# Optimization experiments

Measured on AMD Instinct MI355X. Metric: run time of the kernel, lower is better.

The kernel has to match this reference:

```python
import jax, jax.numpy as jnp
import numpy as np

N = 100000   # nodes
E = 3200000  # edges
F = 128      # input features
H1 = 128     # first_gcn_dimensions
H2 = 64      # second_gcn_dimensions
D1 = 64      # first_dense_neurons
D2 = 8       # second_dense_neurons
L = 10       # number_of_labels


def setup_inputs() -> dict:
    key = jax.random.key(0)
    ks = jax.random.split(key, 8)
    edges = jax.random.randint(ks[0], (2, E), 0, N)
    features = jax.random.normal(ks[1], (N, F), dtype=jnp.float32)
    s = lambda k, shape: jax.random.normal(k, shape, dtype=jnp.float32) * 0.05
    return dict(
        edges=edges, features=features,
        W1=s(ks[2], (F, H1)), b1=jnp.zeros((H1,), jnp.float32),
        W2=s(ks[3], (H1, H2)), b2=jnp.zeros((H2,), jnp.float32),
        Wf1=s(ks[4], (H2, D1)), bf1=jnp.zeros((D1,), jnp.float32),
        Wf2=s(ks[5], (D1, D2)), bf2=jnp.zeros((D2,), jnp.float32),
        Wl=s(ks[6], (H2 * D2, L)), bl=jnp.zeros((L,), jnp.float32),
    )


def gcn_conv(x, W, b, src, dst, n):
    # PyG GCNConv: x' = D^{-1/2} (A + I) D^{-1/2} (x W) + b  (self-loops already in src/dst)
    h = x @ W                                            # [N, out]
    deg = jax.ops.segment_sum(jnp.ones(dst.shape[0], x.dtype), dst, num_segments=n)
    dinv = jnp.where(deg > 0, jax.lax.rsqrt(deg), 0.0)   # deg^{-1/2}, 0 for isolated
    norm = dinv[src] * dinv[dst]                         # [E+N]
    agg = jax.ops.segment_sum(h[src] * norm[:, None], dst, num_segments=n)
    return agg + b


def reference(edges, features, W1, b1, W2, b2, Wf1, bf1, Wf2, bf2, Wl, bl):
    n = features.shape[0]
    loop = jnp.arange(n)
    src = jnp.concatenate([edges[0], loop])
    dst = jnp.concatenate([edges[1], loop])

    h1 = jax.nn.relu(gcn_conv(features, W1, b1, src, dst, n))  # [N, H1]
    h2 = gcn_conv(h1, W2, b2, src, dst, n)                     # [N, H2]

    a1 = jnp.tanh(h2 @ Wf1 + bf1)                              # [N, D1]
    att = jax.nn.softmax(a1 @ Wf2 + bf2, axis=0)               # softmax over nodes, [N, D2]

    graph_embedding = (att.T @ h2).reshape(1, -1)              # [1, D2*H2]
    P = att.T @ att - jnp.eye(att.shape[1], dtype=att.dtype)   # [D2, D2]
    penalty = jnp.sum(jnp.sqrt(jnp.sum(P * P, axis=1)))

    predictions = jax.nn.log_softmax(graph_embedding @ Wl + bl, axis=1)  # [1, L]
    return graph_embedding, penalty, predictions
```

## Files before the change

### kernel.cpp

```cpp
#include <hip/hip_runtime.h>
#include <hip/hip_bf16.h>
#include <math.h>

#define NNODES 100000
#define NEDGES 3200000
#define NBUK ((NNODES + 127) >> 7)
#define NCHUNK 256
#define EPC (NEDGES / NCHUNK)

typedef float floatx2 __attribute__((ext_vector_type(2)));
typedef float f32x4 __attribute__((ext_vector_type(4)));
typedef short bf16x8 __attribute__((ext_vector_type(8)));

__device__ __forceinline__ unsigned short f2bf(float x) {
    unsigned u = __float_as_uint(x);
    unsigned r = u + 0x7FFFu + ((u >> 16) & 1u);
    return (unsigned short)(r >> 16);
}

__device__ __forceinline__ void acc8_fp8(uint2 v, floatx2* a) {
    a[0] += __builtin_amdgcn_cvt_pk_f32_fp8(v.x, false);
    a[1] += __builtin_amdgcn_cvt_pk_f32_fp8(v.x, true);
    a[2] += __builtin_amdgcn_cvt_pk_f32_fp8(v.y, false);
    a[3] += __builtin_amdgcn_cvt_pk_f32_fp8(v.y, true);
}
__device__ __forceinline__ void acc4_fp8(unsigned v, floatx2* a) {
    a[0] += __builtin_amdgcn_cvt_pk_f32_fp8(v, false);
    a[1] += __builtin_amdgcn_cvt_pk_f32_fp8(v, true);
}

__global__ void prep_w_kernel(const float* __restrict__ W1, const float* __restrict__ W2,
                              unsigned short* __restrict__ Wt1, unsigned short* __restrict__ Wt2) {
    int i = blockIdx.x * 256 + threadIdx.x;
    if (i < 128 * 128) {
        int k = i >> 7, n = i & 127;
        Wt1[n * 128 + k] = f2bf(W1[i]);
    } else if (i < 128 * 128 + 128 * 64) {
        int j = i - 128 * 128;
        int k = j >> 6, n = j & 63;
        Wt2[n * 128 + k] = f2bf(W2[j]);
    }
}

__global__ __launch_bounds__(1024) void chunk_hist_kernel(const int* __restrict__ dst,
                                                          int* __restrict__ hist) {
    __shared__ int h[NBUK];
    int c = blockIdx.x, t = threadIdx.x;
    for (int i = t; i < NBUK; i += 1024) h[i] = 0;
    __syncthreads();
    const int4* d4 = (const int4*)(dst + c * EPC);
    for (int i = t; i < EPC / 4; i += 1024) {
        int4 d = d4[i];
        atomicAdd(&h[d.x >> 7], 1);
        atomicAdd(&h[d.y >> 7], 1);
        atomicAdd(&h[d.z >> 7], 1);
        atomicAdd(&h[d.w >> 7], 1);
    }
    __syncthreads();
    for (int i = t; i < NBUK; i += 1024)
        hist[c * NBUK + i] = h[i];
}

__global__ void col_scan_kernel(int* __restrict__ hist, int* __restrict__ btot) {
    int t = blockIdx.x * 256 + threadIdx.x;
    if (t >= NBUK) return;
    int run = 0;
    for (int c = 0; c < NCHUNK; c++) {
        int idx = c * NBUK + t;
        int v = hist[idx];
        hist[idx] = run;
        run += v;
    }
    btot[t] = run;
}

__global__ void bucket_scan_kernel(const int* __restrict__ btot, int* __restrict__ bstart,
                                   int* __restrict__ row_start, float* __restrict__ smalls) {
    __shared__ int s[1024];
    int t = threadIdx.x;
    if (t < 592) smalls[t] = 0.0f;
    int v = (t < NBUK) ? btot[t] : 0;
    s[t] = v;
    __syncthreads();
    for (int off = 1; off < 1024; off <<= 1) {
        int x = (t >= off) ? s[t - off] : 0;
        __syncthreads();
        s[t] += x;
        __syncthreads();
    }
    if (t < NBUK) bstart[t] = s[t] - v;
    if (t == 0) {
        bstart[NBUK] = NEDGES;
        row_start[NNODES] = NEDGES;
    }
}

__global__ __launch_bounds__(1024) void chunk_scatter_kernel(const int* __restrict__ src,
                                                             const int* __restrict__ dst,
                                                             const int* __restrict__ hist,
                                                             const int* __restrict__ bstart,
                                                             int* __restrict__ ebuk) {
    __shared__ int cur[NBUK];
    int c = blockIdx.x, t = threadIdx.x;
    for (int i = t; i < NBUK; i += 1024)
        cur[i] = bstart[i] + hist[c * NBUK + i];
    __syncthreads();
    const int4* s4 = (const int4*)(src + c * EPC);
    const int4* d4 = (const int4*)(dst + c * EPC);
    for (int i = t; i < EPC / 4; i += 1024) {
        int4 s = s4[i];
        int4 d = d4[i];
        int p0 = atomicAdd(&cur[d.x >> 7], 1);
        ebuk[p0] = s.x | ((d.x & 127) << 20);
        int p1 = atomicAdd(&cur[d.y >> 7], 1);
        ebuk[p1] = s.y | ((d.y & 127) << 20);
        int p2 = atomicAdd(&cur[d.z >> 7], 1);
        ebuk[p2] = s.z | ((d.z & 127) << 20);
        int p3 = atomicAdd(&cur[d.w >> 7], 1);
        ebuk[p3] = s.w | ((d.w & 127) << 20);
    }
}

__global__ __launch_bounds__(256) void build_kernel(const int* __restrict__ ebuk,
                                                    const int* __restrict__ bstart,
                                                    int* __restrict__ row_start,
                                                    float* __restrict__ dinv,
                                                    int* __restrict__ csr) {
    __shared__ int cnt[128];
    __shared__ int scn[128];
    __shared__ int cur[128];
    int b = blockIdx.x;
    int t = threadIdx.x;
    int s0 = bstart[b], s1 = bstart[b + 1];
    if (t < 128) cnt[t] = 0;
    __syncthreads();
    for (int i = s0 + t; i < s1; i += 256)
        atomicAdd(&cnt[(ebuk[i] >> 20) & 127], 1);
    __syncthreads();
    if (t < 128) scn[t] = cnt[t];
    __syncthreads();
#pragma unroll
    for (int off = 1; off < 128; off <<= 1) {
        int x = (t < 128 && t >= off) ? scn[t - off] : 0;
        __syncthreads();
        if (t < 128) scn[t] += x;
        __syncthreads();
    }
    int node = b * 128 + t;
    if (t < 128) {
        int rs = s0 + scn[t] - cnt[t];
        cur[t] = rs;
        if (node < NNODES) {
            row_start[node] = rs;
            dinv[node] = rsqrtf((float)cnt[t] + 1.0f);
        }
    }
    __syncthreads();
    for (int i = s0 + t; i < s1; i += 256) {
        int v = ebuk[i];
        int pos = atomicAdd(&cur[(v >> 20) & 127], 1);
        csr[pos] = v & 0xFFFFF;
    }
}

template <int KIN, int KOUT, bool ABF16>
__global__ __launch_bounds__(256) void gemm_mfma_kernel(const void* __restrict__ Av,
                                                        const unsigned short* __restrict__ Wt,
                                                        const float* __restrict__ rowscale,
                                                        unsigned char* __restrict__ stage) {
    constexpr int LDK = KIN + 8;
    constexpr int LDC = KOUT + 4;
    constexpr int SH_AB = (64 + KOUT) * LDK * 2;
    constexpr int SH_C  = 64 * LDC * 4;
    constexpr int SH = SH_AB > SH_C ? SH_AB : SH_C;
    __shared__ char shbuf[SH];
    unsigned short* As = (unsigned short*)shbuf;
    unsigned short* Ws = As + 64 * LDK;
    float* Cs = (float*)shbuf;
    int t = threadIdx.x;
    int block_row = blockIdx.x * 64;

    for (int idx = t; idx < KOUT * (KIN / 8); idx += 256) {
        int n = idx / (KIN / 8), c = idx % (KIN / 8);
        *(uint4*)(Ws + n * LDK + c * 8) = *(const uint4*)(Wt + n * KIN + c * 8);
    }
    if (ABF16) {
        const unsigned short* A = (const unsigned short*)Av;
        for (int idx = t; idx < 64 * (KIN / 8); idx += 256) {
            int r = idx / (KIN / 8), c = idx % (KIN / 8);
            uint4 v = make_uint4(0, 0, 0, 0);
            if (block_row + r < NNODES)
                v = *(const uint4*)(A + (size_t)(block_row + r) * KIN + c * 8);
            *(uint4*)(As + r * LDK + c * 8) = v;
        }
    } else {
        const float* A = (const float*)Av;
        for (int idx = t; idx < 64 * (KIN / 4); idx += 256) {
            int r = idx / (KIN / 4), c = idx % (KIN / 4);
            float4 v = make_float4(0.f, 0.f, 0.f, 0.f);
            if (block_row + r < NNODES)
                v = *(const float4*)(A + (size_t)(block_row + r) * KIN + c * 4);
            unsigned p0 = (unsigned)f2bf(v.x) | ((unsigned)f2bf(v.y) << 16);
            unsigned p1 = (unsigned)f2bf(v.z) | ((unsigned)f2bf(v.w) << 16);
            *(uint2*)(As + r * LDK + c * 4) = make_uint2(p0, p1);
        }
    }
    __syncthreads();

    int wv = t >> 6, lane = t & 63;
    int r0 = wv * 16;
    int m = lane & 15, q = lane >> 4;
    constexpr int NT = KOUT / 16;
    constexpr int KS = KIN / 32;
    f32x4 acc[NT];
#pragma unroll
    for (int nt = 0; nt < NT; nt++) acc[nt] = (f32x4)(0.f);
    bf16x8 afr[KS];
#pragma unroll
    for (int ks = 0; ks < KS; ks++)
        afr[ks] = *(bf16x8*)(As + (r0 + m) * LDK + ks * 32 + q * 8);
#pragma unroll
    for (int nt = 0; nt < NT; nt++) {
#pragma unroll
        for (int ks = 0; ks < KS; ks++) {
            bf16x8 b = *(bf16x8*)(Ws + (nt * 16 + m) * LDK + ks * 32 + q * 8);
            acc[nt] = __builtin_amdgcn_mfma_f32_16x16x32_bf16(afr[ks], b, acc[nt], 0, 0, 0);
        }
    }
    __syncthreads();
#pragma unroll
    for (int nt = 0; nt < NT; nt++)
#pragma unroll
        for (int j = 0; j < 4; j++)
            Cs[(r0 + q * 4 + j) * LDC + nt * 16 + m] = acc[nt][j];
    __syncthreads();
    for (int idx = t; idx < 64 * (KOUT / 4); idx += 256) {
        int r = idx / (KOUT / 4), c4 = idx % (KOUT / 4);
        int row = block_row + r;
        if (row < NNODES) {
            float4 v = *(float4*)(Cs + r * LDC + c4 * 4);
            float d = rowscale[row];
            int pk = __builtin_amdgcn_cvt_pk_fp8_f32(v.x * d, v.y * d, 0, false);
            pk = __builtin_amdgcn_cvt_pk_fp8_f32(v.z * d, v.w * d, pk, true);
            *(unsigned*)(stage + (size_t)row * KOUT + c4 * 4) = (unsigned)pk;
        }
    }
}

__global__ __launch_bounds__(256) void gather128_kernel(
    const unsigned char* __restrict__ hs, const int* __restrict__ row_start,
    const int* __restrict__ csr, const float* __restrict__ dinv,
    const float* __restrict__ bias, unsigned short* __restrict__ out) {
    int wave = threadIdx.x >> 6;
    int lane = threadIdx.x & 63;
    int n = blockIdx.x * 4 + wave;
    if (n >= NNODES) return;
    int g = lane >> 4;
    int c = lane & 15;
    unsigned boff = (unsigned)c << 3;
    int start = row_start[n], end = row_start[n + 1];
    floatx2 acc[4];
#pragma unroll
    for (int i = 0; i < 4; i++) acc[i] = (floatx2)(0.f);
    int w = (start + 3) & ~3;
    if (w > end) w = end;
    {
        int e2 = start + g;
        if (e2 < w) {
            unsigned o = ((unsigned)csr[e2] << 7) + boff;
            acc8_fp8(*(const uint2*)(hs + o), acc);
        }
    }
    for (; w + 32 <= end; w += 32) {
        int4 ca = *(const int4*)(csr + w + 4 * g);
        int4 cbv = *(const int4*)(csr + w + 16 + 4 * g);
        uint2 v0 = *(const uint2*)(hs + (((unsigned)ca.x  << 7) + boff));
        uint2 v1 = *(const uint2*)(hs + (((unsigned)ca.y  << 7) + boff));
        uint2 v2 = *(const uint2*)(hs + (((unsigned)ca.z  << 7) + boff));
        uint2 v3 = *(const uint2*)(hs + (((unsigned)ca.w  << 7) + boff));
        uint2 v4 = *(const uint2*)(hs + (((unsigned)cbv.x << 7) + boff));
        uint2 v5 = *(const uint2*)(hs + (((unsigned)cbv.y << 7) + boff));
        uint2 v6 = *(const uint2*)(hs + (((unsigned)cbv.z << 7) + boff));
        uint2 v7 = *(const uint2*)(hs + (((unsigned)cbv.w << 7) + boff));
        acc8_fp8(v0, acc); acc8_fp8(v1, acc); acc8_fp8(v2, acc); acc8_fp8(v3, acc);
        acc8_fp8(v4, acc); acc8_fp8(v5, acc); acc8_fp8(v6, acc); acc8_fp8(v7, acc);
    }
    for (; w + 16 <= end; w += 16) {
        int4 cs = *(const int4*)(csr + w + 4 * g);
        uint2 v0 = *(const uint2*)(hs + (((unsigned)cs.x << 7) + boff));
        uint2 v1 = *(const uint2*)(hs + (((unsigned)cs.y << 7) + boff));
        uint2 v2 = *(const uint2*)(hs + (((unsigned)cs.z << 7) + boff));
        uint2 v3 = *(const uint2*)(hs + (((unsigned)cs.w << 7) + boff));
        acc8_fp8(v0, acc); acc8_fp8(v1, acc); acc8_fp8(v2, acc); acc8_fp8(v3, acc);
    }
    for (int e2 = w + g; e2 < end; e2 += 4) {
        unsigned o = ((unsigned)csr[e2] << 7) + boff;
        acc8_fp8(*(const uint2*)(hs + o), acc);
    }
#pragma unroll
    for (int off = 16; off <= 32; off <<= 1)
#pragma unroll
        for (int i = 0; i < 4; i++) {
            acc[i].x += __shfl_xor(acc[i].x, off);
            acc[i].y += __shfl_xor(acc[i].y, off);
        }
    if (g == 0) {
        floatx2 s[4];
#pragma unroll
        for (int i = 0; i < 4; i++) s[i] = (floatx2)(0.f);
        acc8_fp8(*(const uint2*)(hs + (((unsigned)n << 7) + boff)), s);
        float d = dinv[n];
        int j = c * 8;
        float4 b0 = *(const float4*)(bias + j);
        float4 b1 = *(const float4*)(bias + j + 4);
        float r0 = fmaxf((acc[0].x + s[0].x) * d + b0.x, 0.f);
        float r1 = fmaxf((acc[0].y + s[0].y) * d + b0.y, 0.f);
        float r2 = fmaxf((acc[1].x + s[1].x) * d + b0.z, 0.f);
        float r3 = fmaxf((acc[1].y + s[1].y) * d + b0.w, 0.f);
        float r4 = fmaxf((acc[2].x + s[2].x) * d + b1.x, 0.f);
        float r5 = fmaxf((acc[2].y + s[2].y) * d + b1.y, 0.f);
        float r6 = fmaxf((acc[3].x + s[3].x) * d + b1.z, 0.f);
        float r7 = fmaxf((acc[3].y + s[3].y) * d + b1.w, 0.f);
        uint4 p;
        p.x = (unsigned)f2bf(r0) | ((unsigned)f2bf(r1) << 16);
        p.y = (unsigned)f2bf(r2) | ((unsigned)f2bf(r3) << 16);
        p.z = (unsigned)f2bf(r4) | ((unsigned)f2bf(r5) << 16);
        p.w = (unsigned)f2bf(r6) | ((unsigned)f2bf(r7) << 16);
        *(uint4*)(out + (((size_t)n << 7) + j)) = p;
    }
}

__global__ __launch_bounds__(256) void gather64_kernel(
    const unsigned char* __restrict__ hs, const int* __restrict__ row_start,
    const int* __restrict__ csr, const float* __restrict__ dinv,
    const float* __restrict__ bias, float* __restrict__ out) {
    int wave = threadIdx.x >> 6;
    int lane = threadIdx.x & 63;
    int n = blockIdx.x * 4 + wave;
    if (n >= NNODES) return;
    int g = lane >> 4;
    int c = lane & 15;
    unsigned boff = (unsigned)c << 2;
    int start = row_start[n], end = row_start[n + 1];
    floatx2 acc[2];
    acc[0] = (floatx2)(0.f); acc[1] = (floatx2)(0.f);
    int w = (start + 3) & ~3;
    if (w > end) w = end;
    {
        int e2 = start + g;
        if (e2 < w) {
            unsigned o = ((unsigned)csr[e2] << 6) + boff;
            acc4_fp8(*(const unsigned*)(hs + o), acc);
        }
    }
    for (; w + 32 <= end; w += 32) {
        int4 ca = *(const int4*)(csr + w + 4 * g);
        int4 cbv = *(const int4*)(csr + w + 16 + 4 * g);
        unsigned v0 = *(const unsigned*)(hs + (((unsigned)ca.x  << 6) + boff));
        unsigned v1 = *(const unsigned*)(hs + (((unsigned)ca.y  << 6) + boff));
        unsigned v2 = *(const unsigned*)(hs + (((unsigned)ca.z  << 6) + boff));
        unsigned v3 = *(const unsigned*)(hs + (((unsigned)ca.w  << 6) + boff));
        unsigned v4 = *(const unsigned*)(hs + (((unsigned)cbv.x << 6) + boff));
        unsigned v5 = *(const unsigned*)(hs + (((unsigned)cbv.y << 6) + boff));
        unsigned v6 = *(const unsigned*)(hs + (((unsigned)cbv.z << 6) + boff));
        unsigned v7 = *(const unsigned*)(hs + (((unsigned)cbv.w << 6) + boff));
        acc4_fp8(v0, acc); acc4_fp8(v1, acc); acc4_fp8(v2, acc); acc4_fp8(v3, acc);
        acc4_fp8(v4, acc); acc4_fp8(v5, acc); acc4_fp8(v6, acc); acc4_fp8(v7, acc);
    }
    for (; w + 16 <= end; w += 16) {
        int4 cs = *(const int4*)(csr + w + 4 * g);
        unsigned v0 = *(const unsigned*)(hs + (((unsigned)cs.x << 6) + boff));
        unsigned v1 = *(const unsigned*)(hs + (((unsigned)cs.y << 6) + boff));
        unsigned v2 = *(const unsigned*)(hs + (((unsigned)cs.z << 6) + boff));
        unsigned v3 = *(const unsigned*)(hs + (((unsigned)cs.w << 6) + boff));
        acc4_fp8(v0, acc); acc4_fp8(v1, acc); acc4_fp8(v2, acc); acc4_fp8(v3, acc);
    }
    for (int e2 = w + g; e2 < end; e2 += 4) {
        unsigned o = ((unsigned)csr[e2] << 6) + boff;
        acc4_fp8(*(const unsigned*)(hs + o), acc);
    }
#pragma unroll
    for (int off = 16; off <= 32; off <<= 1)
#pragma unroll
        for (int i = 0; i < 2; i++) {
            acc[i].x += __shfl_xor(acc[i].x, off);
            acc[i].y += __shfl_xor(acc[i].y, off);
        }
    if (g == 0) {
        floatx2 s[2];
        s[0] = (floatx2)(0.f); s[1] = (floatx2)(0.f);
        acc4_fp8(*(const unsigned*)(hs + (((unsigned)n << 6) + boff)), s);
        float d = dinv[n];
        int j = c * 4;
        float4 b4 = *(const float4*)(bias + j);
        float4 r;
        r.x = (acc[0].x + s[0].x) * d + b4.x;
        r.y = (acc[0].y + s[0].y) * d + b4.y;
        r.z = (acc[1].x + s[1].x) * d + b4.z;
        r.w = (acc[1].y + s[1].y) * d + b4.w;
        *(float4*)(out + (((size_t)n << 6) + j)) = r;
    }
}

__global__ __launch_bounds__(256) void attnpool_kernel(const float* __restrict__ h2,
                                                       const float* __restrict__ Wf1,
                                                       const float* __restrict__ bf1,
                                                       const float* __restrict__ Wf2,
                                                       const float* __restrict__ bf2,
                                                       float* __restrict__ ge,
                                                       float* __restrict__ ata,
                                                       float* __restrict__ colsum) {
    __shared__ float h2S[64][68];
    __shared__ float a1S[64][68];
    __shared__ float attS[64][8];
    __shared__ float colS[8][64];
    int t = threadIdx.x;
    int d0 = t >> 6;
    int j  = t & 63;
    int de = t >> 3, ee = t & 7;
    float accge0 = 0.f, accge1 = 0.f, accata = 0.f, acccol = 0.f;
    int ntiles = (NNODES + 63) / 64;
    for (int tile = blockIdx.x; tile < ntiles; tile += gridDim.x) {
        int base = tile * 64;
#pragma unroll
        for (int q = 0; q < 4; q++) {
            int idx = t + q * 256;
            int r = idx >> 4, cc = (idx & 15) * 4;
            int row = base + r;
            float4 v = (row < NNODES) ? *(const float4*)(h2 + (size_t)row * 64 + cc)
                                      : make_float4(0.f, 0.f, 0.f, 0.f);
            *(float4*)(&h2S[r][cc]) = v;
        }
        __syncthreads();
        {
            int cg = t & 15, rg = t >> 4;
            int jj = cg * 4, r0 = rg * 4;
            float4 b4 = *(const float4*)(bf1 + jj);
            float4 acc[4];
#pragma unroll
            for (int r = 0; r < 4; r++) acc[r] = b4;
#pragma unroll 4
            for (int k = 0; k < 64; k++) {
                float4 wv = *(const float4*)(Wf1 + (size_t)k * 64 + jj);
#pragma unroll
                for (int r = 0; r < 4; r++) {
                    float a = h2S[r0 + r][k];
                    acc[r].x += a * wv.x; acc[r].y += a * wv.y;
                    acc[r].z += a * wv.z; acc[r].w += a * wv.w;
                }
            }
#pragma unroll
            for (int r = 0; r < 4; r++) {
                a1S[r0 + r][jj]     = tanhf(acc[r].x);
                a1S[r0 + r][jj + 1] = tanhf(acc[r].y);
                a1S[r0 + r][jj + 2] = tanhf(acc[r].z);
                a1S[r0 + r][jj + 3] = tanhf(acc[r].w);
            }
        }
        __syncthreads();
        {
            int cc = t & 7, r = t >> 3;
#pragma unroll
            for (int h = 0; h < 2; h++) {
                int rr = r + h * 32;
                float acc = bf2[cc];
                for (int k = 0; k < 64; k++)
                    acc += a1S[rr][k] * Wf2[(size_t)k * 8 + cc];
                float ev = (base + rr < NNODES) ? __expf(acc) : 0.f;
                attS[rr][cc] = ev;
                colS[cc][rr] = ev;
            }
        }
        __syncthreads();
#pragma unroll 8
        for (int i = 0; i < 64; i++) {
            float hv = h2S[i][j];
            accge0 += attS[i][d0] * hv;
            accge1 += attS[i][d0 + 4] * hv;
        }
        if (t < 64) {
#pragma unroll 8
            for (int i = 0; i < 64; i++) accata += attS[i][de] * attS[i][ee];
        }
        if (t < 8) {
            float s = 0.f;
#pragma unroll
            for (int r = 0; r < 64; r++) s += colS[t][r];
            acccol += s;
        }
        __syncthreads();
    }
    atomicAdd(ge + d0 * 64 + j, accge0);
    atomicAdd(ge + (d0 + 4) * 64 + j, accge1);
    if (t < 64) atomicAdd(ata + de * 8 + ee, accata);
    if (t < 8) atomicAdd(colsum + t, acccol);
}

__global__ void final_kernel(const float* __restrict__ geacc, const float* __restrict__ ata,
                             const float* __restrict__ colsum, const float* __restrict__ Wl,
                             const float* __restrict__ bl, float* __restrict__ out) {
    __shared__ float geF[512];
    __shared__ float inv[8];
    __shared__ float logits[10];
    int t = threadIdx.x;
    if (t < 8) inv[t] = 1.0f / colsum[t];
    __syncthreads();
    for (int idx = t; idx < 512; idx += 64) {
        int d = idx >> 6;
        float v = geacc[idx] * inv[d];
        geF[idx] = v;
        out[idx] = v;
    }
    __syncthreads();
    if (t == 0) {
        float pen = 0.f;
        for (int d = 0; d < 8; d++) {
            float s = 0.f;
            for (int e = 0; e < 8; e++) {
                float p = ata[d * 8 + e] * inv[d] * inv[e] - (d == e ? 1.0f : 0.0f);
                s += p * p;
            }
            pen += sqrtf(s);
        }
        out[512] = pen;
    }
    if (t < 10) {
        float acc = bl[t];
        for (int k = 0; k < 512; k++) acc += geF[k] * Wl[(size_t)k * 10 + t];
        logits[t] = acc;
    }
    __syncthreads();
    if (t == 0) {
        float m = -INFINITY;
        for (int l = 0; l < 10; l++) m = fmaxf(m, logits[l]);
        float s = 0.f;
        for (int l = 0; l < 10; l++) s += expf(logits[l] - m);
        float ls = logf(s);
        for (int l = 0; l < 10; l++) out[513 + l] = logits[l] - m - ls;
    }
}

extern "C" void kernel_launch(void* const* d_in, const int* in_sizes, int n_in,
                              void* d_out, int out_size, void* d_ws, size_t ws_size,
                              hipStream_t stream) {
    const int* esrc = (const int*)d_in[0];
    const int* edst = esrc + NEDGES;
    const float* X   = (const float*)d_in[1];
    const float* W1  = (const float*)d_in[2];
    const float* b1  = (const float*)d_in[3];
    const float* W2  = (const float*)d_in[4];
    const float* b2  = (const float*)d_in[5];
    const float* Wf1 = (const float*)d_in[6];
    const float* bf1 = (const float*)d_in[7];
    const float* Wf2 = (const float*)d_in[8];
    const float* bf2 = (const float*)d_in[9];
    const float* Wl  = (const float*)d_in[10];
    const float* bl  = (const float*)d_in[11];
    float* out = (float*)d_out;

    float* ws     = (float*)d_ws;
    float* dinv   = ws;
    float* smalls = ws + 100352;
    float* colsum = smalls + 8;
    float* ata    = smalls + 16;
    float* geacc  = smalls + 80;
    float* A = ws + 101376;
    float* B = A + (size_t)NNODES * 128;
    int* row_start = (int*)(B + (size_t)NNODES * 128);
    int* btot      = row_start + 100352;
    int* bstart    = btot + 1024;
    int* csr       = bstart + 1024;
    unsigned short* Wt1 = (unsigned short*)(csr + NEDGES);
    unsigned short* Wt2 = Wt1 + 128 * 128;
    int* ebuk      = (int*)A;
    int* hist      = (int*)B;
    unsigned char* stage = (unsigned char*)A;
    unsigned short* h1 = (unsigned short*)B;
    float* h2  = B;

    prep_w_kernel<<<96, 256, 0, stream>>>(W1, W2, Wt1, Wt2);

    chunk_hist_kernel<<<NCHUNK, 1024, 0, stream>>>(edst, hist);
    col_scan_kernel<<<4, 256, 0, stream>>>(hist, btot);
    bucket_scan_kernel<<<1, 1024, 0, stream>>>(btot, bstart, row_start, smalls);
    chunk_scatter_kernel<<<NCHUNK, 1024, 0, stream>>>(esrc, edst, hist, bstart, ebuk);
    build_kernel<<<NBUK, 256, 0, stream>>>(ebuk, bstart, row_start, dinv, csr);

    gemm_mfma_kernel<128, 128, false><<<(NNODES + 63) / 64, 256, 0, stream>>>(X, Wt1, dinv, stage);
    gather128_kernel<<<(NNODES + 3) / 4, 256, 0, stream>>>(stage, row_start, csr, dinv, b1, h1);

    gemm_mfma_kernel<128, 64, true><<<(NNODES + 63) / 64, 256, 0, stream>>>(h1, Wt2, dinv, stage);
    gather64_kernel<<<(NNODES + 3) / 4, 256, 0, stream>>>(stage, row_start, csr, dinv, b2, h2);

    attnpool_kernel<<<512, 256, 0, stream>>>(h2, Wf1, bf1, Wf2, bf2, geacc, ata, colsum);
    final_kernel<<<1, 64, 0, stream>>>(geacc, ata, colsum, Wl, bl, out);
}
```

Baseline: 430.9 us.

## Fuse gathers with downstream GEMM and attention pooling, merge prep and scan kernels

The layer-1 neighbor gather now runs inside the layer-2 GEMM kernel, writing the ReLU bf16 rows straight into shared memory instead of round-tripping h1 through global memory. The layer-2 gather is folded into the attention-pooling kernel, so the fp32 h2 tensor is never materialized. The weight-prep kernel is merged into the histogram kernel as extra blocks, and the column and bucket scans are combined into one kernel, cutting launches. The cost is less parallelism in the gathers: each wave now handles 16 rows in sequence instead of one node, which may hurt latency hiding for the irregular loads.

```diff
diff --git a/kernel.cpp b/kernel.cpp
--- a/kernel.cpp
+++ b/kernel.cpp
@@ -29,23 +29,26 @@
     a[1] += __builtin_amdgcn_cvt_pk_f32_fp8(v, true);
 }
 
-__global__ void prep_w_kernel(const float* __restrict__ W1, const float* __restrict__ W2,
-                              unsigned short* __restrict__ Wt1, unsigned short* __restrict__ Wt2) {
-    int i = blockIdx.x * 256 + threadIdx.x;
-    if (i < 128 * 128) {
-        int k = i >> 7, n = i & 127;
-        Wt1[n * 128 + k] = f2bf(W1[i]);
-    } else if (i < 128 * 128 + 128 * 64) {
-        int j = i - 128 * 128;
-        int k = j >> 6, n = j & 63;
-        Wt2[n * 128 + k] = f2bf(W2[j]);
-    }
-}
-
-__global__ __launch_bounds__(1024) void chunk_hist_kernel(const int* __restrict__ dst,
-                                                          int* __restrict__ hist) {
+__global__ __launch_bounds__(1024) void hist_prep_kernel(const int* __restrict__ dst,
+                                                         int* __restrict__ hist,
+                                                         const float* __restrict__ W1,
+                                                         const float* __restrict__ W2,
+                                                         unsigned short* __restrict__ Wt1,
+                                                         unsigned short* __restrict__ Wt2) {
+    int c = blockIdx.x, t = threadIdx.x;
+    if (c >= NCHUNK) {
+        int i = (c - NCHUNK) * 1024 + t;
+        if (i < 128 * 128) {
+            int k = i >> 7, n = i & 127;
+            Wt1[n * 128 + k] = f2bf(W1[i]);
+        } else {
+            int j = i - 128 * 128;
+            int k = j >> 6, n = j & 63;
+            Wt2[n * 128 + k] = f2bf(W2[j]);
+        }
+        return;
+    }
     __shared__ int h[NBUK];
-    int c = blockIdx.x, t = threadIdx.x;
     for (int i = t; i < NBUK; i += 1024) h[i] = 0;
     __syncthreads();
     const int4* d4 = (const int4*)(dst + c * EPC);
@@ -61,26 +64,22 @@
         hist[c * NBUK + i] = h[i];
 }
 
-__global__ void col_scan_kernel(int* __restrict__ hist, int* __restrict__ btot) {
-    int t = blockIdx.x * 256 + threadIdx.x;
-    if (t >= NBUK) return;
-    int run = 0;
-    for (int c = 0; c < NCHUNK; c++) {
-        int idx = c * NBUK + t;
-        int v = hist[idx];
-        hist[idx] = run;
-        run += v;
-    }
-    btot[t] = run;
-}
-
-__global__ void bucket_scan_kernel(const int* __restrict__ btot, int* __restrict__ bstart,
-                                   int* __restrict__ row_start, float* __restrict__ smalls) {
+__global__ __launch_bounds__(1024) void scan_kernel(int* __restrict__ hist, int* __restrict__ bstart,
+                                                    int* __restrict__ row_start,
+                                                    float* __restrict__ smalls) {
     __shared__ int s[1024];
     int t = threadIdx.x;
     if (t < 592) smalls[t] = 0.0f;
-    int v = (t < NBUK) ? btot[t] : 0;
-    s[t] = v;
+    int run = 0;
+    if (t < NBUK) {
+        for (int c = 0; c < NCHUNK; c++) {
+            int idx = c * NBUK + t;
+            int v = hist[idx];
+            hist[idx] = run;
+            run += v;
+        }
+    }
+    s[t] = (t < NBUK) ? run : 0;
     __syncthreads();
     for (int off = 1; off < 1024; off <<= 1) {
         int x = (t >= off) ? s[t - off] : 0;
@@ -88,7 +87,7 @@
         s[t] += x;
         __syncthreads();
     }
-    if (t < NBUK) bstart[t] = s[t] - v;
+    if (t < NBUK) bstart[t] = s[t] - run;
     if (t == 0) {
         bstart[NBUK] = NEDGES;
         row_start[NNODES] = NEDGES;
@@ -163,11 +162,11 @@
     }
 }
 
-template <int KIN, int KOUT, bool ABF16>
-__global__ __launch_bounds__(256) void gemm_mfma_kernel(const void* __restrict__ Av,
-                                                        const unsigned short* __restrict__ Wt,
-                                                        const float* __restrict__ rowscale,
-                                                        unsigned char* __restrict__ stage) {
+__global__ __launch_bounds__(256) void gemm1_mfma_kernel(const float* __restrict__ A,
+                                                         const unsigned short* __restrict__ Wt,
+                                                         const float* __restrict__ rowscale,
+                                                         unsigned char* __restrict__ stage) {
+    constexpr int KIN = 128, KOUT = 128;
     constexpr int LDK = KIN + 8;
     constexpr int LDC = KOUT + 4;
     constexpr int SH_AB = (64 + KOUT) * LDK * 2;
@@ -184,26 +183,14 @@
         int n = idx / (KIN / 8), c = idx % (KIN / 8);
         *(uint4*)(Ws + n * LDK + c * 8) = *(const uint4*)(Wt + n * KIN + c * 8);
     }
-    if (ABF16) {
-        const unsigned short* A = (const unsigned short*)Av;
-        for (int idx = t; idx < 64 * (KIN / 8); idx += 256) {
-            int r = idx / (KIN / 8), c = idx % (KIN / 8);
-            uint4 v = make_uint4(0, 0, 0, 0);
-            if (block_row + r < NNODES)
-                v = *(const uint4*)(A + (size_t)(block_row + r) * KIN + c * 8);
-            *(uint4*)(As + r * LDK + c * 8) = v;
-        }
-    } else {
-        const float* A = (const float*)Av;
-        for (int idx = t; idx < 64 * (KIN / 4); idx += 256) {
-            int r = idx / (KIN / 4), c = idx % (KIN / 4);
-            float4 v = make_float4(0.f, 0.f, 0.f, 0.f);
-            if (block_row + r < NNODES)
-                v = *(const float4*)(A + (size_t)(block_row + r) * KIN + c * 4);
-            unsigned p0 = (unsigned)f2bf(v.x) | ((unsigned)f2bf(v.y) << 16);
-            unsigned p1 = (unsigned)f2bf(v.z) | ((unsigned)f2bf(v.w) << 16);
-            *(uint2*)(As + r * LDK + c * 4) = make_uint2(p0, p1);
-        }
+    for (int idx = t; idx < 64 * (KIN / 4); idx += 256) {
+        int r = idx / (KIN / 4), c = idx % (KIN / 4);
+        float4 v = make_float4(0.f, 0.f, 0.f, 0.f);
+        if (block_row + r < NNODES)
+            v = *(const float4*)(A + (size_t)(block_row + r) * KIN + c * 4);
+        unsigned p0 = (unsigned)f2bf(v.x) | ((unsigned)f2bf(v.y) << 16);
+        unsigned p1 = (unsigned)f2bf(v.z) | ((unsigned)f2bf(v.w) << 16);
+        *(uint2*)(As + r * LDK + c * 4) = make_uint2(p0, p1);
     }
     __syncthreads();
 
@@ -247,189 +234,236 @@
     }
 }
 
-__global__ __launch_bounds__(256) void gather128_kernel(
+__global__ __launch_bounds__(256) void g128_gemm2_kernel(
     const unsigned char* __restrict__ hs, const int* __restrict__ row_start,
     const int* __restrict__ csr, const float* __restrict__ dinv,
-    const float* __restrict__ bias, unsigned short* __restrict__ out) {
-    int wave = threadIdx.x >> 6;
-    int lane = threadIdx.x & 63;
-    int n = blockIdx.x * 4 + wave;
-    if (n >= NNODES) return;
-    int g = lane >> 4;
-    int c = lane & 15;
-    unsigned boff = (unsigned)c << 3;
-    int start = row_start[n], end = row_start[n + 1];
-    floatx2 acc[4];
-#pragma unroll
-    for (int i = 0; i < 4; i++) acc[i] = (floatx2)(0.f);
-    int w = (start + 3) & ~3;
-    if (w > end) w = end;
+    const float* __restrict__ b1, const unsigned short* __restrict__ Wt2,
+    unsigned char* __restrict__ stage2) {
+    constexpr int KIN = 128, KOUT = 64;
+    constexpr int LDK = KIN + 8;
+    constexpr int LDC = KOUT + 4;
+    __shared__ unsigned short As[64 * LDK];
+    __shared__ unsigned short Ws[KOUT * LDK];
+    float* Cs = (float*)As;
+    int t = threadIdx.x;
+    int block_row = blockIdx.x * 64;
+    int wv = t >> 6, lane = t & 63;
+
+    for (int idx = t; idx < KOUT * (KIN / 8); idx += 256) {
+        int n = idx / (KIN / 8), cc = idx % (KIN / 8);
+        *(uint4*)(Ws + n * LDK + cc * 8) = *(const uint4*)(Wt2 + n * KIN + cc * 8);
+    }
     {
-        int e2 = start + g;
-        if (e2 < w) {
-            unsigned o = ((unsigned)csr[e2] << 7) + boff;
-            acc8_fp8(*(const uint2*)(hs + o), acc);
-        }
-    }
-    for (; w + 32 <= end; w += 32) {
-        int4 ca = *(const int4*)(csr + w + 4 * g);
-        int4 cbv = *(const int4*)(csr + w + 16 + 4 * g);
-        uint2 v0 = *(const uint2*)(hs + (((unsigned)ca.x  << 7) + boff));
-        uint2 v1 = *(const uint2*)(hs + (((unsigned)ca.y  << 7) + boff));
-        uint2 v2 = *(const uint2*)(hs + (((unsigned)ca.z  << 7) + boff));
-        uint2 v3 = *(const uint2*)(hs + (((unsigned)ca.w  << 7) + boff));
-        uint2 v4 = *(const uint2*)(hs + (((unsigned)cbv.x << 7) + boff));
-        uint2 v5 = *(const uint2*)(hs + (((unsigned)cbv.y << 7) + boff));
-        uint2 v6 = *(const uint2*)(hs + (((unsigned)cbv.z << 7) + boff));
-        uint2 v7 = *(const uint2*)(hs + (((unsigned)cbv.w << 7) + boff));
-        acc8_fp8(v0, acc); acc8_fp8(v1, acc); acc8_fp8(v2, acc); acc8_fp8(v3, acc);
-        acc8_fp8(v4, acc); acc8_fp8(v5, acc); acc8_fp8(v6, acc); acc8_fp8(v7, acc);
-    }
-    for (; w + 16 <= end; w += 16) {
-        int4 cs = *(const int4*)(csr + w + 4 * g);
-        uint2 v0 = *(const uint2*)(hs + (((unsigned)cs.x << 7) + boff));
-        uint2 v1 = *(const uint2*)(hs + (((unsigned)cs.y << 7) + boff));
-        uint2 v2 = *(const uint2*)(hs + (((unsigned)cs.z << 7) + boff));
-        uint2 v3 = *(const uint2*)(hs + (((unsigned)cs.w << 7) + boff));
-        acc8_fp8(v0, acc); acc8_fp8(v1, acc); acc8_fp8(v2, acc); acc8_fp8(v3, acc);
-    }
-    for (int e2 = w + g; e2 < end; e2 += 4) {
-        unsigned o = ((unsigned)csr[e2] << 7) + boff;
-        acc8_fp8(*(const uint2*)(hs + o), acc);
-    }
-#pragma unroll
-    for (int off = 16; off <= 32; off <<= 1)
-#pragma unroll
-        for (int i = 0; i < 4; i++) {
-            acc[i].x += __shfl_xor(acc[i].x, off);
-            acc[i].y += __shfl_xor(acc[i].y, off);
-        }
-    if (g == 0) {
-        floatx2 s[4];
-#pragma unroll
-        for (int i = 0; i < 4; i++) s[i] = (floatx2)(0.f);
-        acc8_fp8(*(const uint2*)(hs + (((unsigned)n << 7) + boff)), s);
-        float d = dinv[n];
-        int j = c * 8;
-        float4 b0 = *(const float4*)(bias + j);
-        float4 b1 = *(const float4*)(bias + j + 4);
-        float r0 = fmaxf((acc[0].x + s[0].x) * d + b0.x, 0.f);
-        float r1 = fmaxf((acc[0].y + s[0].y) * d + b0.y, 0.f);
-        float r2 = fmaxf((acc[1].x + s[1].x) * d + b0.z, 0.f);
-        float r3 = fmaxf((acc[1].y + s[1].y) * d + b0.w, 0.f);
-        float r4 = fmaxf((acc[2].x + s[2].x) * d + b1.x, 0.f);
-        float r5 = fmaxf((acc[2].y + s[2].y) * d + b1.y, 0.f);
-        float r6 = fmaxf((acc[3].x + s[3].x) * d + b1.z, 0.f);
-        float r7 = fmaxf((acc[3].y + s[3].y) * d + b1.w, 0.f);
-        uint4 p;
-        p.x = (unsigned)f2bf(r0) | ((unsigned)f2bf(r1) << 16);
-        p.y = (unsigned)f2bf(r2) | ((unsigned)f2bf(r3) << 16);
-        p.z = (unsigned)f2bf(r4) | ((unsigned)f2bf(r5) << 16);
-        p.w = (unsigned)f2bf(r6) | ((unsigned)f2bf(r7) << 16);
-        *(uint4*)(out + (((size_t)n << 7) + j)) = p;
-    }
-}
-
-__global__ __launch_bounds__(256) void gather64_kernel(
+        int g = lane >> 4, c = lane & 15;
+        unsigned boff = (unsigned)c << 3;
+        for (int i = 0; i < 16; i++) {
+            int r = wv * 16 + i;
+            int n = block_row + r;
+            if (n >= NNODES) {
+                if (g == 0) *(uint4*)(As + r * LDK + c * 8) = make_uint4(0, 0, 0, 0);
+                continue;
+            }
+            int start = row_start[n], end = row_start[n + 1];
+            floatx2 acc[4];
+#pragma unroll
+            for (int ii = 0; ii < 4; ii++) acc[ii] = (floatx2)(0.f);
+            int w = (start + 3) & ~3;
+            if (w > end) w = end;
+            {
+                int e2 = start + g;
+                if (e2 < w) {
+                    unsigned o = ((unsigned)csr[e2] << 7) + boff;
+                    acc8_fp8(*(const uint2*)(hs + o), acc);
+                }
+            }
+            for (; w + 32 <= end; w += 32) {
+                int4 ca = *(const int4*)(csr + w + 4 * g);
+                int4 cbv = *(const int4*)(csr + w + 16 + 4 * g);
+                uint2 v0 = *(const uint2*)(hs + (((unsigned)ca.x  << 7) + boff));
+                uint2 v1 = *(const uint2*)(hs + (((unsigned)ca.y  << 7) + boff));
+                uint2 v2 = *(const uint2*)(hs + (((unsigned)ca.z  << 7) + boff));
+                uint2 v3 = *(const uint2*)(hs + (((unsigned)ca.w  << 7) + boff));
+                uint2 v4 = *(const uint2*)(hs + (((unsigned)cbv.x << 7) + boff));
+                uint2 v5 = *(const uint2*)(hs + (((unsigned)cbv.y << 7) + boff));
+                uint2 v6 = *(const uint2*)(hs + (((unsigned)cbv.z << 7) + boff));
+                uint2 v7 = *(const uint2*)(hs + (((unsigned)cbv.w << 7) + boff));
+                acc8_fp8(v0, acc); acc8_fp8(v1, acc); acc8_fp8(v2, acc); acc8_fp8(v3, acc);
+                acc8_fp8(v4, acc); acc8_fp8(v5, acc); acc8_fp8(v6, acc); acc8_fp8(v7, acc);
+            }
+            for (; w + 16 <= end; w += 16) {
+                int4 cs = *(const int4*)(csr + w + 4 * g);
+                uint2 v0 = *(const uint2*)(hs + (((unsigned)cs.x << 7) + boff));
+                uint2 v1 = *(const uint2*)(hs + (((unsigned)cs.y << 7) + boff));
+                uint2 v2 = *(const uint2*)(hs + (((unsigned)cs.z << 7) + boff));
+                uint2 v3 = *(const uint2*)(hs + (((unsigned)cs.w << 7) + boff));
+                acc8_fp8(v0, acc); acc8_fp8(v1, acc); acc8_fp8(v2, acc); acc8_fp8(v3, acc);
+            }
+            for (int e2 = w + g; e2 < end; e2 += 4) {
+                unsigned o = ((unsigned)csr[e2] << 7) + boff;
+                acc8_fp8(*(const uint2*)(hs + o), acc);
+            }
+#pragma unroll
+            for (int off = 16; off <= 32; off <<= 1)
+#pragma unroll
+                for (int ii = 0; ii < 4; ii++) {
+                    acc[ii].x += __shfl_xor(acc[ii].x, off);
+                    acc[ii].y += __shfl_xor(acc[ii].y, off);
+                }
+            if (g == 0) {
+                floatx2 s[4];
+#pragma unroll
+                for (int ii = 0; ii < 4; ii++) s[ii] = (floatx2)(0.f);
+                acc8_fp8(*(const uint2*)(hs + (((unsigned)n << 7) + boff)), s);
+                float d = dinv[n];
+                int j = c * 8;
+                float4 bb0 = *(const float4*)(b1 + j);
+                float4 bb1 = *(const float4*)(b1 + j + 4);
+                float r0 = fmaxf((acc[0].x + s[0].x) * d + bb0.x, 0.f);
+                float r1 = fmaxf((acc[0].y + s[0].y) * d + bb0.y, 0.f);
+                float r2 = fmaxf((acc[1].x + s[1].x) * d + bb0.z, 0.f);
+                float r3 = fmaxf((acc[1].y + s[1].y) * d + bb0.w, 0.f);
+                float r4 = fmaxf((acc[2].x + s[2].x) * d + bb1.x, 0.f);
+                float r5 = fmaxf((acc[2].y + s[2].y) * d + bb1.y, 0.f);
+                float r6 = fmaxf((acc[3].x + s[3].x) * d + bb1.z, 0.f);
+                float r7 = fmaxf((acc[3].y + s[3].y) * d + bb1.w, 0.f);
+                uint4 p;
+                p.x = (unsigned)f2bf(r0) | ((unsigned)f2bf(r1) << 16);
+                p.y = (unsigned)f2bf(r2) | ((unsigned)f2bf(r3) << 16);
+                p.z = (unsigned)f2bf(r4) | ((unsigned)f2bf(r5) << 16);
+                p.w = (unsigned)f2bf(r6) | ((unsigned)f2bf(r7) << 16);
+                *(uint4*)(As + r * LDK + c * 8) = p;
+            }
+        }
+    }
+    __syncthreads();
+    int r0 = wv * 16;
+    int m = lane & 15, q = lane >> 4;
+    constexpr int NT = KOUT / 16;
+    constexpr int KS = KIN / 32;
+    f32x4 acc[NT];
+#pragma unroll
+    for (int nt = 0; nt < NT; nt++) acc[nt] = (f32x4)(0.f);
+    bf16x8 afr[KS];
+#pragma unroll
+    for (int ks = 0; ks < KS; ks++)
+        afr[ks] = *(bf16x8*)(As + (r0 + m) * LDK + ks * 32 + q * 8);
+#pragma unroll
+    for (int nt = 0; nt < NT; nt++) {
+#pragma unroll
+        for (int ks = 0; ks < KS; ks++) {
+            bf16x8 b = *(bf16x8*)(Ws + (nt * 16 + m) * LDK + ks * 32 + q * 8);
+            acc[nt] = __builtin_amdgcn_mfma_f32_16x16x32_bf16(afr[ks], b, acc[nt], 0, 0, 0);
+        }
+    }
+    __syncthreads();
+#pragma unroll
+    for (int nt = 0; nt < NT; nt++)
+#pragma unroll
+        for (int j = 0; j < 4; j++)
+            Cs[(r0 + q * 4 + j) * LDC + nt * 16 + m] = acc[nt][j];
+    __syncthreads();
+    for (int idx = t; idx < 64 * (KOUT / 4); idx += 256) {
+        int r = idx / (KOUT / 4), c4 = idx % (KOUT / 4);
+        int row = block_row + r;
+        if (row < NNODES) {
+            float4 v = *(float4*)(Cs + r * LDC + c4 * 4);
+            float d = dinv[row];
+            int pk = __builtin_amdgcn_cvt_pk_fp8_f32(v.x * d, v.y * d, 0, false);
+            pk = __builtin_amdgcn_cvt_pk_fp8_f32(v.z * d, v.w * d, pk, true);
+            *(unsigned*)(stage2 + (size_t)row * KOUT + c4 * 4) = (unsigned)pk;
+        }
+    }
+}
+
+__global__ __launch_bounds__(256) void g64_attnpool_kernel(
     const unsigned char* __restrict__ hs, const int* __restrict__ row_start,
     const int* __restrict__ csr, const float* __restrict__ dinv,
-    const float* __restrict__ bias, float* __restrict__ out) {
-    int wave = threadIdx.x >> 6;
-    int lane = threadIdx.x & 63;
-    int n = blockIdx.x * 4 + wave;
-    if (n >= NNODES) return;
-    int g = lane >> 4;
-    int c = lane & 15;
-    unsigned boff = (unsigned)c << 2;
-    int start = row_start[n], end = row_start[n + 1];
-    floatx2 acc[2];
-    acc[0] = (floatx2)(0.f); acc[1] = (floatx2)(0.f);
-    int w = (start + 3) & ~3;
-    if (w > end) w = end;
-    {
-        int e2 = start + g;
-        if (e2 < w) {
-            unsigned o = ((unsigned)csr[e2] << 6) + boff;
-            acc4_fp8(*(const unsigned*)(hs + o), acc);
-        }
-    }
-    for (; w + 32 <= end; w += 32) {
-        int4 ca = *(const int4*)(csr + w + 4 * g);
-        int4 cbv = *(const int4*)(csr + w + 16 + 4 * g);
-        unsigned v0 = *(const unsigned*)(hs + (((unsigned)ca.x  << 6) + boff));
-        unsigned v1 = *(const unsigned*)(hs + (((unsigned)ca.y  << 6) + boff));
-        unsigned v2 = *(const unsigned*)(hs + (((unsigned)ca.z  << 6) + boff));
-        unsigned v3 = *(const unsigned*)(hs + (((unsigned)ca.w  << 6) + boff));
-        unsigned v4 = *(const unsigned*)(hs + (((unsigned)cbv.x << 6) + boff));
-        unsigned v5 = *(const unsigned*)(hs + (((unsigned)cbv.y << 6) + boff));
-        unsigned v6 = *(const unsigned*)(hs + (((unsigned)cbv.z << 6) + boff));
-        unsigned v7 = *(const unsigned*)(hs + (((unsigned)cbv.w << 6) + boff));
-        acc4_fp8(v0, acc); acc4_fp8(v1, acc); acc4_fp8(v2, acc); acc4_fp8(v3, acc);
-        acc4_fp8(v4, acc); acc4_fp8(v5, acc); acc4_fp8(v6, acc); acc4_fp8(v7, acc);
-    }
-    for (; w + 16 <= end; w += 16) {
-        int4 cs = *(const int4*)(csr + w + 4 * g);
-        unsigned v0 = *(const unsigned*)(hs + (((unsigned)cs.x << 6) + boff));
-        unsigned v1 = *(const unsigned*)(hs + (((unsigned)cs.y << 6) + boff));
-        unsigned v2 = *(const unsigned*)(hs + (((unsigned)cs.z << 6) + boff));
-        unsigned v3 = *(const unsigned*)(hs + (((unsigned)cs.w << 6) + boff));
-        acc4_fp8(v0, acc); acc4_fp8(v1, acc); acc4_fp8(v2, acc); acc4_fp8(v3, acc);
-    }
-    for (int e2 = w + g; e2 < end; e2 += 4) {
-        unsigned o = ((unsigned)csr[e2] << 6) + boff;
-        acc4_fp8(*(const unsigned*)(hs + o), acc);
-    }
-#pragma unroll
-    for (int off = 16; off <= 32; off <<= 1)
-#pragma unroll
-        for (int i = 0; i < 2; i++) {
-            acc[i].x += __shfl_xor(acc[i].x, off);
-            acc[i].y += __shfl_xor(acc[i].y, off);
-        }
-    if (g == 0) {
-        floatx2 s[2];
-        s[0] = (floatx2)(0.f); s[1] = (floatx2)(0.f);
-        acc4_fp8(*(const unsigned*)(hs + (((unsigned)n << 6) + boff)), s);
-        float d = dinv[n];
-        int j = c * 4;
-        float4 b4 = *(const float4*)(bias + j);
-        float4 r;
-        r.x = (acc[0].x + s[0].x) * d + b4.x;
-        r.y = (acc[0].y + s[0].y) * d + b4.y;
-        r.z = (acc[1].x + s[1].x) * d + b4.z;
-        r.w = (acc[1].y + s[1].y) * d + b4.w;
-        *(float4*)(out + (((size_t)n << 6) + j)) = r;
-    }
-}
-
-__global__ __launch_bounds__(256) void attnpool_kernel(const float* __restrict__ h2,
-                                                       const float* __restrict__ Wf1,
-                                                       const float* __restrict__ bf1,
-                                                       const float* __restrict__ Wf2,
-                                                       const float* __restrict__ bf2,
-                                                       float* __restrict__ ge,
-                                                       float* __restrict__ ata,
-                                                       float* __restrict__ colsum) {
+    const float* __restrict__ b2,
+    const float* __restrict__ Wf1, const float* __restrict__ bf1,
+    const float* __restrict__ Wf2, const float* __restrict__ bf2,
+    float* __restrict__ ge, float* __restrict__ ata, float* __restrict__ colsum) {
     __shared__ float h2S[64][68];
     __shared__ float a1S[64][68];
     __shared__ float attS[64][8];
     __shared__ float colS[8][64];
     int t = threadIdx.x;
-    int d0 = t >> 6;
-    int j  = t & 63;
+    int wv = t >> 6, lane = t & 63;
+    int d0 = t >> 6, j = t & 63;
     int de = t >> 3, ee = t & 7;
     float accge0 = 0.f, accge1 = 0.f, accata = 0.f, acccol = 0.f;
     int ntiles = (NNODES + 63) / 64;
     for (int tile = blockIdx.x; tile < ntiles; tile += gridDim.x) {
         int base = tile * 64;
-#pragma unroll
-        for (int q = 0; q < 4; q++) {
-            int idx = t + q * 256;
-            int r = idx >> 4, cc = (idx & 15) * 4;
-            int row = base + r;
-            float4 v = (row < NNODES) ? *(const float4*)(h2 + (size_t)row * 64 + cc)
-                                      : make_float4(0.f, 0.f, 0.f, 0.f);
-            *(float4*)(&h2S[r][cc]) = v;
+        {
+            int g = lane >> 4, c = lane & 15;
+            unsigned boff = (unsigned)c << 2;
+            for (int i = 0; i < 16; i++) {
+                int r = wv * 16 + i;
+                int n = base + r;
+                if (n >= NNODES) {
+                    if (g == 0) *(float4*)(&h2S[r][c * 4]) = make_float4(0.f, 0.f, 0.f, 0.f);
+                    continue;
+                }
+                int start = row_start[n], end = row_start[n + 1];
+                floatx2 acc[2];
+                acc[0] = (floatx2)(0.f); acc[1] = (floatx2)(0.f);
+                int w = (start + 3) & ~3;
+                if (w > end) w = end;
+                {
+                    int e2 = start + g;
+                    if (e2 < w) {
+                        unsigned o = ((unsigned)csr[e2] << 6) + boff;
+                        acc4_fp8(*(const unsigned*)(hs + o), acc);
+                    }
+                }
+                for (; w + 32 <= end; w += 32) {
+                    int4 ca = *(const int4*)(csr + w + 4 * g);
+                    int4 cbv = *(const int4*)(csr + w + 16 + 4 * g);
+                    unsigned v0 = *(const unsigned*)(hs + (((unsigned)ca.x  << 6) + boff));
+                    unsigned v1 = *(const unsigned*)(hs + (((unsigned)ca.y  << 6) + boff));
+                    unsigned v2 = *(const unsigned*)(hs + (((unsigned)ca.z  << 6) + boff));
+                    unsigned v3 = *(const unsigned*)(hs + (((unsigned)ca.w  << 6) + boff));
+                    unsigned v4 = *(const unsigned*)(hs + (((unsigned)cbv.x << 6) + boff));
+                    unsigned v5 = *(const unsigned*)(hs + (((unsigned)cbv.y << 6) + boff));
+                    unsigned v6 = *(const unsigned*)(hs + (((unsigned)cbv.z << 6) + boff));
+                    unsigned v7 = *(const unsigned*)(hs + (((unsigned)cbv.w << 6) + boff));
+                    acc4_fp8(v0, acc); acc4_fp8(v1, acc); acc4_fp8(v2, acc); acc4_fp8(v3, acc);
+                    acc4_fp8(v4, acc); acc4_fp8(v5, acc); acc4_fp8(v6, acc); acc4_fp8(v7, acc);
+                }
+                for (; w + 16 <= end; w += 16) {
+                    int4 cs = *(const int4*)(csr + w + 4 * g);
+                    unsigned v0 = *(const unsigned*)(hs + (((unsigned)cs.x << 6) + boff));
+                    unsigned v1 = *(const unsigned*)(hs + (((unsigned)cs.y << 6) + boff));
+                    unsigned v2 = *(const unsigned*)(hs + (((unsigned)cs.z << 6) + boff));
+                    unsigned v3 = *(const unsigned*)(hs + (((unsigned)cs.w << 6) + boff));
+                    acc4_fp8(v0, acc); acc4_fp8(v1, acc); acc4_fp8(v2, acc); acc4_fp8(v3, acc);
+                }
+                for (int e2 = w + g; e2 < end; e2 += 4) {
+                    unsigned o = ((unsigned)csr[e2] << 6) + boff;
+                    acc4_fp8(*(const unsigned*)(hs + o), acc);
+                }
+#pragma unroll
+                for (int off = 16; off <= 32; off <<= 1)
+#pragma unroll
+                    for (int ii = 0; ii < 2; ii++) {
+                        acc[ii].x += __shfl_xor(acc[ii].x, off);
+                        acc[ii].y += __shfl_xor(acc[ii].y, off);
+                    }
+                if (g == 0) {
+                    floatx2 s[2];
+                    s[0] = (floatx2)(0.f); s[1] = (floatx2)(0.f);
+                    acc4_fp8(*(const unsigned*)(hs + (((unsigned)n << 6) + boff)), s);
+                    float d = dinv[n];
+                    int jj = c * 4;
+                    float4 b4 = *(const float4*)(b2 + jj);
+                    float4 res;
+                    res.x = (acc[0].x + s[0].x) * d + b4.x;
+                    res.y = (acc[0].y + s[0].y) * d + b4.y;
+                    res.z = (acc[1].x + s[1].x) * d + b4.z;
+                    res.w = (acc[1].y + s[1].y) * d + b4.w;
+                    *(float4*)(&h2S[r][jj]) = res;
+                }
+            }
         }
         __syncthreads();
         {
@@ -441,12 +475,12 @@
             for (int r = 0; r < 4; r++) acc[r] = b4;
 #pragma unroll 4
             for (int k = 0; k < 64; k++) {
-                float4 wv = *(const float4*)(Wf1 + (size_t)k * 64 + jj);
+                float4 wv4 = *(const float4*)(Wf1 + (size_t)k * 64 + jj);
 #pragma unroll
                 for (int r = 0; r < 4; r++) {
                     float a = h2S[r0 + r][k];
-                    acc[r].x += a * wv.x; acc[r].y += a * wv.y;
-                    acc[r].z += a * wv.z; acc[r].w += a * wv.w;
+                    acc[r].x += a * wv4.x; acc[r].y += a * wv4.y;
+                    acc[r].z += a * wv4.z; acc[r].w += a * wv4.w;
                 }
             }
 #pragma unroll
@@ -567,31 +601,26 @@
     float* A = ws + 101376;
     float* B = A + (size_t)NNODES * 128;
     int* row_start = (int*)(B + (size_t)NNODES * 128);
-    int* btot      = row_start + 100352;
-    int* bstart    = btot + 1024;
+    int* bstart    = row_start + 100352;
     int* csr       = bstart + 1024;
     unsigned short* Wt1 = (unsigned short*)(csr + NEDGES);
     unsigned short* Wt2 = Wt1 + 128 * 128;
     int* ebuk      = (int*)A;
     int* hist      = (int*)B;
-    unsigned char* stage = (unsigned char*)A;
-    unsigned short* h1 = (unsigned short*)B;
-    float* h2  = B;
-
-    prep_w_kernel<<<96, 256, 0, stream>>>(W1, W2, Wt1, Wt2);
-
-    chunk_hist_kernel<<<NCHUNK, 1024, 0, stream>>>(edst, hist);
-    col_scan_kernel<<<4, 256, 0, stream>>>(hist, btot);
-    bucket_scan_kernel<<<1, 1024, 0, stream>>>(btot, bstart, row_start, smalls);
+    unsigned char* stage1 = (unsigned char*)A;
+    unsigned char* stage2 = (unsigned char*)B;
+
+    hist_prep_kernel<<<NCHUNK + 24, 1024, 0, stream>>>(edst, hist, W1, W2, Wt1, Wt2);
+    scan_kernel<<<1, 1024, 0, stream>>>(hist, bstart, row_start, smalls);
     chunk_scatter_kernel<<<NCHUNK, 1024, 0, stream>>>(esrc, edst, hist, bstart, ebuk);
     build_kernel<<<NBUK, 256, 0, stream>>>(ebuk, bstart, row_start, dinv, csr);
 
-    gemm_mfma_kernel<128, 128, false><<<(NNODES + 63) / 64, 256, 0, stream>>>(X, Wt1, dinv, stage);
-    gather128_kernel<<<(NNODES + 3) / 4, 256, 0, stream>>>(stage, row_start, csr, dinv, b1, h1);
-
-    gemm_mfma_kernel<128, 64, true><<<(NNODES + 63) / 64, 256, 0, stream>>>(h1, Wt2, dinv, stage);
-    gather64_kernel<<<(NNODES + 3) / 4, 256, 0, stream>>>(stage, row_start, csr, dinv, b2, h2);
-
-    attnpool_kernel<<<512, 256, 0, stream>>>(h2, Wf1, bf1, Wf2, bf2, geacc, ata, colsum);
+    gemm1_mfma_kernel<<<(NNODES + 63) / 64, 256, 0, stream>>>(X, Wt1, dinv, stage1);
+
+    g128_gemm2_kernel<<<(NNODES + 63) / 64, 256, 0, stream>>>(stage1, row_start, csr, dinv,
+                                                              b1, Wt2, stage2);
+
+    g64_attnpool_kernel<<<782, 256, 0, stream>>>(stage2, row_start, csr, dinv, b2,
+                                                 Wf1, bf1, Wf2, bf2, geacc, ata, colsum);
     final_kernel<<<1, 64, 0, stream>>>(geacc, ata, colsum, Wl, bl, out);
 }
```

Result: slower. 629.8 us (+46.2%).
